# Kernel optimization log

Measured on AMD Instinct MI355X. Metric: run time of the kernel, lower is better.

Reference implementation:

```python
import jax, jax.numpy as jnp
import numpy as np


def setup_inputs() -> dict:
    key = jax.random.key(0)
    k1, k2, k3 = jax.random.split(key, 3)
    RAW_NODES = 40962          # ico-6 sphere
    NUM_NODES = RAW_NODES * 4 - 6   # 163842, ico-7 sphere
    FEAT = 256
    x = jax.random.normal(k1, (RAW_NODES, FEAT), dtype=jnp.float32)
    max_index = jax.random.randint(k2, (RAW_NODES, FEAT), 0, 7, dtype=jnp.int64)
    neigh_orders = jax.random.randint(k3, (RAW_NODES * 7,), 0, NUM_NODES, dtype=jnp.int64)
    return {"x": x, "max_index": max_index, "neigh_orders": neigh_orders, "num_nodes": NUM_NODES}


def reference(x, max_index, neigh_orders, num_nodes):
    raw_nodes, feat_num = x.shape
    # column_ref[i, f] = i*7 + max_index[i, f]  (vectorized form of the python loop)
    column_ref = (jnp.arange(raw_nodes, dtype=max_index.dtype)[:, None] * 7 + max_index).reshape(-1)
    column_index = neigh_orders[column_ref]  # gather from neighborhood lookup table
    # row_index exactly as in the original: floor(linspace(0, feat_num, raw_nodes*feat_num)), last clamped
    row_index = np.floor(np.linspace(0.0, float(feat_num), num=raw_nodes * feat_num)).astype(np.int64)
    row_index[-1] = row_index[-1] - 1
    row_index = jnp.asarray(row_index)
    y = jnp.zeros((num_nodes, feat_num), dtype=x.dtype)
    # scatter: y[column_index, row_index] = x.view(-1)
    y = y.at[column_index, row_index].set(x.reshape(-1))
    return y
```

## Files before the change

### kernel.cpp

```cpp
#include <hip/hip_runtime.h>
#include <hip/hip_cooperative_groups.h>
#include <stdint.h>

namespace cg = cooperative_groups;


#define FEAT 256
#define LOG2FEAT 8
#define HASH_BITS 12
#define HASH_SIZE (1 << HASH_BITS)
#define HASH_MASK (HASH_SIZE - 1)
#define BLOCK 1024
#define MAX_WIN_NODES 164

__device__ __forceinline__ void hash_insert(int* h_key, int* h_val, int col, int k) {
    unsigned h = ((unsigned)col * 2654435761u) >> (32 - HASH_BITS);
    for (;;) {
        int cur = h_key[h];
        if (cur == -1) {
            cur = atomicCAS(&h_key[h], -1, col);
            if (cur == -1) cur = col;
        }
        if (cur == col) {
            atomicMax(&h_val[h], k);
            return;
        }
        h = (h + 1) & HASH_MASK;
    }
}

__global__ void __launch_bounds__(BLOCK)
upsample_fused_kernel(const float* __restrict__ x,
                      const int*   __restrict__ mi,
                      const int*   __restrict__ neigh,
                      float*       __restrict__ out,
                      int total,
                      int out_elems)
{
    __shared__ int h_key[HASH_SIZE];
    __shared__ int h_val[HASH_SIZE];
    __shared__ int neigh_lds[MAX_WIN_NODES * 7];

    const int r   = blockIdx.x;
    const int tid = threadIdx.x;

    const long long tm1 = (long long)total - 1;
    const int k_lo = (int)(((long long)r * tm1 + (FEAT - 1)) >> LOG2FEAT);
    int       k_hi = (int)(((long long)(r + 1) * tm1 + (FEAT - 1)) >> LOG2FEAT);
    if (r == FEAT - 1) k_hi = total;

    const int i_lo = k_lo >> LOG2FEAT;
    const int i_hi = (k_hi - 1) >> LOG2FEAT;
    const int nwin7 = (i_hi - i_lo + 1) * 7;

    for (int idx = tid; idx < HASH_SIZE; idx += BLOCK) {
        h_key[idx] = -1;
        h_val[idx] = 0;
    }
    for (int idx = tid; idx < nwin7; idx += BLOCK)
        neigh_lds[idx] = neigh[i_lo * 7 + idx];
    __syncthreads();

    const int lane        = tid & 63;
    const int f           = tid & (FEAT - 1);
    const int wave_f_base = tid & (FEAT - 1) & ~63;
    const int node_off    = tid >> LOG2FEAT;

    for (int ibase = i_lo; ibase <= i_hi; ibase += (BLOCK >> LOG2FEAT)) {
        const int i = ibase + node_off;
        const int k = (i << LOG2FEAT) | f;
        const bool valid = (i <= i_hi) && (k >= k_lo) && (k < k_hi);
        const int m = valid ? mi[k] : 7;

        const unsigned long long b0 = __ballot(m == 0);
        const unsigned long long b1 = __ballot(m == 1);
        const unsigned long long b2 = __ballot(m == 2);
        const unsigned long long b3 = __ballot(m == 3);
        const unsigned long long b4 = __ballot(m == 4);
        const unsigned long long b5 = __ballot(m == 5);
        const unsigned long long b6 = __ballot(m == 6);
        unsigned long long mym =
            (lane == 0) ? b0 : (lane == 1) ? b1 : (lane == 2) ? b2 :
            (lane == 3) ? b3 : (lane == 4) ? b4 : (lane == 5) ? b5 :
            (lane == 6) ? b6 : 0ull;
        if (mym != 0ull) {
            const int top  = 63 - __clzll(mym);
            const int k_t  = (i << LOG2FEAT) | (wave_f_base + top);
            const int col  = neigh_lds[(i - i_lo) * 7 + lane];
            hash_insert(h_key, h_val, col, k_t);
        }
    }

    float4* out4 = (float4*)out;
    const int total4 = out_elems >> 2;
    const float4 z = make_float4(0.f, 0.f, 0.f, 0.f);
    for (int idx = blockIdx.x * BLOCK + tid; idx < total4; idx += gridDim.x * BLOCK)
        out4[idx] = z;

    cg::this_grid().sync();

    for (int idx = tid; idx < HASH_SIZE; idx += BLOCK) {
        const int col = h_key[idx];
        if (col >= 0)
            out[(size_t)col << LOG2FEAT | (size_t)r] = x[h_val[idx]];
    }
}

extern "C" void kernel_launch(void* const* d_in, const int* in_sizes, int n_in,
                              void* d_out, int out_size, void* d_ws, size_t ws_size,
                              hipStream_t stream) {
    const float* x     = (const float*)d_in[0];
    const int*   mi    = (const int*)d_in[1];
    const int*   neigh = (const int*)d_in[2];
    float*       out   = (float*)d_out;

    int total     = in_sizes[0];
    int out_elems = out_size;

    void* args[] = { (void*)&x, (void*)&mi, (void*)&neigh, (void*)&out,
                     (void*)&total, (void*)&out_elems };
    hipLaunchCooperativeKernel((const void*)upsample_fused_kernel,
                               dim3(FEAT), dim3(BLOCK), args, 0, stream);
}
```

Before: 336.3 us.

## Split cooperative kernel into build/zero kernel plus drain kernel via workspace

```diff
diff --git a/kernel.cpp b/kernel.cpp
--- a/kernel.cpp
+++ b/kernel.cpp
@@ -1,8 +1,5 @@
 #include <hip/hip_runtime.h>
-#include <hip/hip_cooperative_groups.h>
 #include <stdint.h>
-
-namespace cg = cooperative_groups;
 
 
 #define FEAT 256
@@ -11,7 +8,11 @@
 #define HASH_SIZE (1 << HASH_BITS)
 #define HASH_MASK (HASH_SIZE - 1)
 #define BLOCK 1024
+#define BUILD_WGS 256
+#define ZERO_WGS 768
 #define MAX_WIN_NODES 164
+#define ENTRY_CAP 1152
+#define ENTRY_BASE_BYTES 4096
 
 __device__ __forceinline__ void hash_insert(int* h_key, int* h_val, int col, int k) {
     unsigned h = ((unsigned)col * 2654435761u) >> (32 - HASH_BITS);
@@ -29,20 +30,34 @@
     }
 }
 
-__global__ void __launch_bounds__(BLOCK)
-upsample_fused_kernel(const float* __restrict__ x,
-                      const int*   __restrict__ mi,
-                      const int*   __restrict__ neigh,
-                      float*       __restrict__ out,
-                      int total,
-                      int out_elems)
+extern "C" __global__ __launch_bounds__(BLOCK)
+void build_zero_kernel(const float* __restrict__ x,
+                       const int*   __restrict__ mi,
+                       const int*   __restrict__ neigh,
+                       float*       __restrict__ out,
+                       int*         __restrict__ ws_counts,
+                       int2*        __restrict__ ws_entries,
+                       int total,
+                       int out_elems)
 {
+    const int tid = threadIdx.x;
+
+    if (blockIdx.x >= BUILD_WGS) {
+        const int zid = blockIdx.x - BUILD_WGS;
+        float4* out4 = (float4*)out;
+        const int total4 = out_elems >> 2;
+        const float4 z = make_float4(0.f, 0.f, 0.f, 0.f);
+        for (int idx = zid * BLOCK + tid; idx < total4; idx += ZERO_WGS * BLOCK)
+            out4[idx] = z;
+        return;
+    }
+
     __shared__ int h_key[HASH_SIZE];
     __shared__ int h_val[HASH_SIZE];
     __shared__ int neigh_lds[MAX_WIN_NODES * 7];
+    __shared__ int lds_count;
 
-    const int r   = blockIdx.x;
-    const int tid = threadIdx.x;
+    const int r = blockIdx.x;
 
     const long long tm1 = (long long)total - 1;
     const int k_lo = (int)(((long long)r * tm1 + (FEAT - 1)) >> LOG2FEAT);
@@ -59,50 +74,72 @@
     }
     for (int idx = tid; idx < nwin7; idx += BLOCK)
         neigh_lds[idx] = neigh[i_lo * 7 + idx];
+    if (tid == 0) lds_count = 0;
     __syncthreads();
 
     const int lane        = tid & 63;
     const int f           = tid & (FEAT - 1);
-    const int wave_f_base = tid & (FEAT - 1) & ~63;
+    const int wave_f_base = f & ~63;
     const int node_off    = tid >> LOG2FEAT;
+
+    int i0 = i_lo + node_off;
+    int k0 = (i0 << LOG2FEAT) | f;
+    bool v0 = (i0 <= i_hi) && (k0 >= k_lo) && (k0 < k_hi);
+    int m_cur = v0 ? mi[k0] : 7;
 
     for (int ibase = i_lo; ibase <= i_hi; ibase += (BLOCK >> LOG2FEAT)) {
         const int i = ibase + node_off;
-        const int k = (i << LOG2FEAT) | f;
-        const bool valid = (i <= i_hi) && (k >= k_lo) && (k < k_hi);
-        const int m = valid ? mi[k] : 7;
 
-        const unsigned long long b0 = __ballot(m == 0);
-        const unsigned long long b1 = __ballot(m == 1);
-        const unsigned long long b2 = __ballot(m == 2);
-        const unsigned long long b3 = __ballot(m == 3);
-        const unsigned long long b4 = __ballot(m == 4);
-        const unsigned long long b5 = __ballot(m == 5);
-        const unsigned long long b6 = __ballot(m == 6);
+        const int ibase_n = ibase + (BLOCK >> LOG2FEAT);
+        const int i_n = ibase_n + node_off;
+        const int k_n = (i_n << LOG2FEAT) | f;
+        const bool v_n = (ibase_n <= i_hi) && (i_n <= i_hi) && (k_n >= k_lo) && (k_n < k_hi);
+        const int m_next = v_n ? mi[k_n] : 7;
+
+        const unsigned long long b0 = __ballot(m_cur == 0);
+        const unsigned long long b1 = __ballot(m_cur == 1);
+        const unsigned long long b2 = __ballot(m_cur == 2);
+        const unsigned long long b3 = __ballot(m_cur == 3);
+        const unsigned long long b4 = __ballot(m_cur == 4);
+        const unsigned long long b5 = __ballot(m_cur == 5);
+        const unsigned long long b6 = __ballot(m_cur == 6);
         unsigned long long mym =
             (lane == 0) ? b0 : (lane == 1) ? b1 : (lane == 2) ? b2 :
             (lane == 3) ? b3 : (lane == 4) ? b4 : (lane == 5) ? b5 :
             (lane == 6) ? b6 : 0ull;
         if (mym != 0ull) {
-            const int top  = 63 - __clzll(mym);
-            const int k_t  = (i << LOG2FEAT) | (wave_f_base + top);
-            const int col  = neigh_lds[(i - i_lo) * 7 + lane];
+            const int top = 63 - __clzll(mym);
+            const int k_t = (i << LOG2FEAT) | (wave_f_base + top);
+            const int col = neigh_lds[(i - i_lo) * 7 + lane];
             hash_insert(h_key, h_val, col, k_t);
         }
+        m_cur = m_next;
     }
-
-    float4* out4 = (float4*)out;
-    const int total4 = out_elems >> 2;
-    const float4 z = make_float4(0.f, 0.f, 0.f, 0.f);
-    for (int idx = blockIdx.x * BLOCK + tid; idx < total4; idx += gridDim.x * BLOCK)
-        out4[idx] = z;
-
-    cg::this_grid().sync();
+    __syncthreads();
 
     for (int idx = tid; idx < HASH_SIZE; idx += BLOCK) {
         const int col = h_key[idx];
-        if (col >= 0)
-            out[(size_t)col << LOG2FEAT | (size_t)r] = x[h_val[idx]];
+        if (col >= 0) {
+            const float v = x[h_val[idx]];
+            const int pos = atomicAdd(&lds_count, 1);
+            if (pos < ENTRY_CAP)
+                ws_entries[r * ENTRY_CAP + pos] = make_int2(col, __float_as_int(v));
+        }
+    }
+    __syncthreads();
+    if (tid == 0) ws_counts[r] = lds_count;
+}
+
+extern "C" __global__ __launch_bounds__(256)
+void drain_kernel(float* __restrict__ out,
+                  const int*  __restrict__ ws_counts,
+                  const int2* __restrict__ ws_entries)
+{
+    const int r = blockIdx.x;
+    const int cnt = ws_counts[r];
+    for (int idx = threadIdx.x; idx < cnt; idx += 256) {
+        const int2 e = ws_entries[r * ENTRY_CAP + idx];
+        out[((size_t)e.x << LOG2FEAT) | (size_t)r] = __int_as_float(e.y);
     }
 }
 
@@ -117,8 +154,10 @@
     int total     = in_sizes[0];
     int out_elems = out_size;
 
-    void* args[] = { (void*)&x, (void*)&mi, (void*)&neigh, (void*)&out,
-                     (void*)&total, (void*)&out_elems };
-    hipLaunchCooperativeKernel((const void*)upsample_fused_kernel,
-                               dim3(FEAT), dim3(BLOCK), args, 0, stream);
+    int*  ws_counts  = (int*)d_ws;
+    int2* ws_entries = (int2*)((char*)d_ws + ENTRY_BASE_BYTES);
+
+    build_zero_kernel<<<dim3(BUILD_WGS + ZERO_WGS), dim3(BLOCK), 0, stream>>>(
+        x, mi, neigh, out, ws_counts, ws_entries, total, out_elems);
+    drain_kernel<<<dim3(FEAT), dim3(256), 0, stream>>>(out, ws_counts, ws_entries);
 }
```

After: 287.6 us. 1.17x faster.
